# Kernel optimization log

Hardware: AMD Instinct MI355X
Metric: run time of the kernel (lower is better)

## Reference

```python
import jax, jax.numpy as jnp
import numpy as np

B, L, D, R = 8, 2048, 2048, 256
K = R if R % 2 == 1 else (R - 1 if R > 1 else 1)  # torch kernel-size rule -> 255


def setup_inputs() -> dict:
    key = jax.random.key(0)
    ks = jax.random.split(key, 6)
    x = jax.random.normal(ks[0], (B, L, D), dtype=jnp.float32)
    ln_gamma = jnp.ones((D,), jnp.float32)
    ln_beta = jnp.zeros((D,), jnp.float32)
    P_shared = jax.random.normal(ks[1], (D, R), jnp.float32) / np.float32(np.sqrt(D))
    dlt_T = jax.random.normal(ks[2], (R, R), jnp.float32) / np.float32(np.sqrt(R))
    phi_w = jax.random.normal(ks[3], (R,), jnp.float32)  # nn.Linear(1, r, bias=False) weight
    phi_bias = jnp.zeros((L, R), jnp.float32)            # created as zeros_like(phi_det)
    toep_params = jnp.ones((K,), jnp.float32) / np.float32(K)
    Wq = jax.random.normal(ks[4], (R, D), jnp.float32) / np.float32(np.sqrt(R))  # delta_Q: r->d
    bq = jnp.zeros((D,), jnp.float32)
    g_logit = jnp.array([-1.0, 0.0], jnp.float32)
    return {"x": x, "ln_gamma": ln_gamma, "ln_beta": ln_beta, "P_shared": P_shared,
            "dlt_T": dlt_T, "phi_w": phi_w, "phi_bias": phi_bias,
            "toep_params": toep_params, "Wq": Wq, "bq": bq, "g_logit": g_logit,
            "step": 5000}


def _layernorm(x, g, b, eps=1e-5):
    m = jnp.mean(x, -1, keepdims=True)
    v = jnp.mean((x - m) ** 2, -1, keepdims=True)
    return (x - m) * jax.lax.rsqrt(v + eps) * g + b


def _phi_det(Ll, Rr, dtype):
    # assumed phi_logic(t, L, r): DCT-II style deterministic phase table, shape (L, r)
    t = jnp.arange(Ll, dtype=dtype)[:, None]
    k = jnp.arange(Rr, dtype=dtype)[None, :]
    return jnp.cos(jnp.pi * (t + 0.5) * k / Ll)


def reference(x, ln_gamma, ln_beta, P_shared, dlt_T, phi_w, phi_bias,
              toep_params, Wq, bq, g_logit, step):
    Bb, Ll, Dd = x.shape
    Rr = P_shared.shape[1]
    x_norm = _layernorm(x, ln_gamma, ln_beta)
    phi_det = _phi_det(Ll, Rr, x.dtype)                      # (L, r)
    feat = jnp.mean(x_norm, -1, keepdims=True)               # (B, L, 1)
    phi_data = jnp.mean(feat * phi_w[None, None, :], axis=0)  # (L, r)
    det_scale = min(step / 2000.0, 1.0)                      # static Python scalar
    phi = det_scale * phi_det + phi_bias + phi_data          # (L, r)
    scale = jnp.sum(phi, axis=1) / jnp.float32(Rr)           # (L,)
    u = jnp.einsum('bld,dr->blr', x_norm, P_shared)          # SharedProj.forward_P
    z = jnp.einsum('blr,sr->bls', u, dlt_T)                  # DLT: fixed spectral transform
    # Toeplitz conv1d across spectral channels, padding 'same' (cross-correlation, as torch)
    zf = z.reshape(Bb * Ll, 1, Rr)
    mixed = jax.lax.conv_general_dilated(zf, toep_params[None, None, :], (1,), 'SAME',
                                         dimension_numbers=('NCH', 'OIH', 'NCH'))
    z_mixed = mixed.reshape(Bb, Ll, Rr)
    y = jnp.einsum('blr,rd->bld', z_mixed, Wq) + bq          # delta_Q
    g = jax.nn.sigmoid(g_logit)
    g = jnp.repeat(g, Dd // g.shape[0])                      # repeat_interleave to d_model
    # scale has L elements, broadcast over the FEATURE dim (L == d_model by construction)
    return g[None, None, :] * y * scale[None, None, :]
```

## Files before the change

kernel.cpp:

```cpp
#include <hip/hip_runtime.h>
#include <cstdint>
#include <math.h>

#define B_ 8
#define L_ 2048
#define D_ 2048
#define R_ 256

typedef __bf16 bf16x8 __attribute__((ext_vector_type(8)));
typedef float f32x4 __attribute__((ext_vector_type(4)));

__device__ __forceinline__ unsigned short f2bf(float f) {
    uint32_t u = __builtin_bit_cast(uint32_t, f);
    u += 0x7FFFu + ((u >> 16) & 1u);
    return (unsigned short)(u >> 16);
}

#define GLDS16(gp, lp)                                                          \
    __builtin_amdgcn_global_load_lds(                                           \
        (const __attribute__((address_space(1))) void*)(gp),                    \
        (__attribute__((address_space(3))) void*)(lp), 16, 0, 0)

__global__ __launch_bounds__(256) void ln_kernel(
    const float* __restrict__ x, const float* __restrict__ gamma,
    const float* __restrict__ beta, unsigned short* __restrict__ xn,
    float* __restrict__ feat)
{
    const int row  = blockIdx.x;
    const int t    = threadIdx.x;
    const int w    = t >> 6, lane = t & 63;
    const float4* x4 = (const float4*)(x + (size_t)row * D_);
    const float4* g4 = (const float4*)gamma;
    const float4* b4 = (const float4*)beta;
    float4 a  = x4[t];
    float4 b  = x4[t + 256];
    float4 g0 = g4[t], g1 = g4[t + 256];
    float4 e0 = b4[t], e1 = b4[t + 256];

    float s   = a.x + a.y + a.z + a.w + b.x + b.y + b.z + b.w;
    float sq  = a.x*a.x + a.y*a.y + a.z*a.z + a.w*a.w
              + b.x*b.x + b.y*b.y + b.z*b.z + b.w*b.w;
    float sxg = a.x*g0.x + a.y*g0.y + a.z*g0.z + a.w*g0.w
              + b.x*g1.x + b.y*g1.y + b.z*g1.z + b.w*g1.w;
    float sg  = g0.x + g0.y + g0.z + g0.w + g1.x + g1.y + g1.z + g1.w;
    float sb  = e0.x + e0.y + e0.z + e0.w + e1.x + e1.y + e1.z + e1.w;

    __shared__ float red[20];
#pragma unroll
    for (int o = 32; o; o >>= 1) {
        s   += __shfl_down(s, o);
        sq  += __shfl_down(sq, o);
        sxg += __shfl_down(sxg, o);
        sg  += __shfl_down(sg, o);
        sb  += __shfl_down(sb, o);
    }
    if (lane == 0) {
        red[w] = s; red[4+w] = sq; red[8+w] = sxg; red[12+w] = sg; red[16+w] = sb;
    }
    __syncthreads();
    float S    = red[0] + red[1] + red[2] + red[3];
    float SQ   = red[4] + red[5] + red[6] + red[7];
    float SXG  = red[8] + red[9] + red[10] + red[11];
    float SG   = red[12] + red[13] + red[14] + red[15];
    float SB   = red[16] + red[17] + red[18] + red[19];
    float mean = S * (1.0f / D_);
    float var  = SQ * (1.0f / D_) - mean * mean;
    float rstd = rsqrtf(var + 1e-5f);
    if (t == 0)
        feat[row] = (rstd * (SXG - mean * SG) + SB) * (1.0f / D_);

    float n[8];
    n[0] = (a.x - mean) * rstd * g0.x + e0.x;
    n[1] = (a.y - mean) * rstd * g0.y + e0.y;
    n[2] = (a.z - mean) * rstd * g0.z + e0.z;
    n[3] = (a.w - mean) * rstd * g0.w + e0.w;
    n[4] = (b.x - mean) * rstd * g1.x + e1.x;
    n[5] = (b.y - mean) * rstd * g1.y + e1.y;
    n[6] = (b.z - mean) * rstd * g1.z + e1.z;
    n[7] = (b.w - mean) * rstd * g1.w + e1.w;

    ushort4 o0, o1;
    o0.x = f2bf(n[0]); o0.y = f2bf(n[1]); o0.z = f2bf(n[2]); o0.w = f2bf(n[3]);
    o1.x = f2bf(n[4]); o1.y = f2bf(n[5]); o1.z = f2bf(n[6]); o1.w = f2bf(n[7]);
    ((ushort4*)(xn + (size_t)row * D_))[t]       = o0;
    ((ushort4*)(xn + (size_t)row * D_))[t + 256] = o1;
}

__global__ __launch_bounds__(256) void prep1_kernel(
    const float* __restrict__ P, unsigned short* __restrict__ PT,
    const float* __restrict__ toep, const float* __restrict__ Wq,
    float* __restrict__ C,
    const float* __restrict__ phi_bias, const float* __restrict__ phi_w,
    const float* __restrict__ feat, const float* __restrict__ bq,
    const float* __restrict__ g_logit, const int* __restrict__ step,
    float* __restrict__ gs, float* __restrict__ bgs)
{
    __shared__ __align__(16) char smem[32768];
    const int bid = blockIdx.x;
    const int t   = threadIdx.x;

    if (bid < 32) {
        unsigned short* sT = (unsigned short*)smem;
        const int k0 = bid * 64;
#pragma unroll 8
        for (int j = 0; j < 64; j++)
            sT[j * 256 + t] = f2bf(P[(size_t)(k0 + j) * R_ + t]);
        __syncthreads();
#pragma unroll
        for (int c = 0; c < 16; c++) {
            ushort4 v;
            v.x = sT[(c * 4 + 0) * 256 + t];
            v.y = sT[(c * 4 + 1) * 256 + t];
            v.z = sT[(c * 4 + 2) * 256 + t];
            v.w = sT[(c * 4 + 3) * 256 + t];
            *(ushort4*)(PT + (size_t)t * D_ + k0 + c * 4) = v;
        }
    } else if (bid < 160) {
        float* T2 = (float*)smem;
        const int cid = bid - 32;
        const int r0  = (cid >> 3) * 16;
        const int d   = (cid & 7) * 256 + t;
        {
            int j0 = t - 128;
            T2[t] = ((unsigned)j0 < 255u) ? toep[j0] : 0.f;
            int j1 = t + 128;
            T2[t + 256] = ((unsigned)j1 < 255u) ? toep[j1] : 0.f;
        }
        __syncthreads();
        float acc[16] = {};
#pragma unroll 4
        for (int s = 0; s < 256; s++) {
            float wv = Wq[(size_t)s * D_ + d];
            int base = r0 - s + 255;
#pragma unroll
            for (int ri = 0; ri < 16; ri++)
                acc[ri] += T2[base + ri] * wv;
        }
#pragma unroll
        for (int ri = 0; ri < 16; ri++)
            C[(size_t)(r0 + ri) * D_ + d] = acc[ri];
    } else {
        float* redp = (float*)smem;
        const int l0   = (bid - 160) * 32;
        const int w    = t >> 6, lane = t & 63;
        float pw = phi_w[t];
#pragma unroll
        for (int o = 32; o; o >>= 1) pw += __shfl_down(pw, o);
        if (lane == 0) redp[w] = pw;
        __syncthreads();
        float pws = redp[0] + redp[1] + redp[2] + redp[3];
        float det = fminf((float)step[0] / 2000.0f, 1.0f);
        float fscl = pws * (1.0f / B_);
#pragma unroll
        for (int i = 0; i < 8; i++) {
            int l = l0 + w * 8 + i;
            float4 pv = *(const float4*)(phi_bias + (size_t)l * R_ + lane * 4);
            float val = pv.x + pv.y + pv.z + pv.w;
            if (lane < 8) val += feat[(size_t)lane * L_ + l] * fscl;
#pragma unroll
            for (int o = 32; o; o >>= 1) val += __shfl_down(val, o);
            if (lane == 0) {
                float a  = 3.14159265358979323846f * ((float)l + 0.5f) * (1.0f / L_);
                float cs = sinf(128.0f * a) * cosf(127.5f * a) / sinf(0.5f * a);
                float sc = (det * cs + val) * (1.0f / R_);
                float gl = g_logit[l >> 10];
                float gg = 1.0f / (1.0f + expf(-gl));
                gs[l]  = gg * sc;
                bgs[l] = bq[l] * gg * sc;
            }
        }
    }
}

__global__ __launch_bounds__(256) void prep2_kernel(
    const float* __restrict__ dlt, const float* __restrict__ C,
    unsigned short* __restrict__ WT)
{
    const int d0 = blockIdx.x * 2;
    const int q  = threadIdx.x;
    float a0 = 0.f, a1 = 0.f;
#pragma unroll 8
    for (int r = 0; r < 256; r++) {
        float dv = dlt[(size_t)r * R_ + q];
        const float* cr = C + (size_t)r * D_ + d0;
        a0 += dv * cr[0];
        a1 += dv * cr[1];
    }
    WT[(size_t)(d0 + 0) * R_ + q] = f2bf(a0);
    WT[(size_t)(d0 + 1) * R_ + q] = f2bf(a1);
}

__global__ __launch_bounds__(256, 2) void gemm1_kernel(
    const unsigned short* __restrict__ A,
    const unsigned short* __restrict__ BT,
    unsigned short* __restrict__ U)
{
    __shared__ __align__(16) unsigned short sA[2][2][128 * 32];
    __shared__ __align__(16) unsigned short sB[2][2][128 * 32];
    const int tid  = threadIdx.x;
    const int n0   = blockIdx.x * 128;
    const int m0   = blockIdx.y * 128;
    const int w    = tid >> 6, lane = tid & 63;
    const int quad = lane >> 4, m16 = lane & 15;
    const int wm   = (w >> 1) * 64, wn = (w & 1) * 64;
    const int ra   = tid >> 2, sa = tid & 3;

    const unsigned short* apb = A  + (size_t)(m0 + ra) * 2048 + sa * 8;
    const unsigned short* bpb = BT + (size_t)(n0 + ra) * 2048 + sa * 8;

    f32x4 acc[4][4] = {};

#define G1_STAGE(buf, kc)                                                       \
    do {                                                                        \
        _Pragma("unroll")                                                       \
        for (int h = 0; h < 2; h++) {                                           \
            GLDS16(apb + (kc) + h * 32,              &sA[buf][h][tid * 8]);     \
            GLDS16(apb + (kc) + h * 32 + 64 * 2048,  &sA[buf][h][2048 + tid * 8]); \
            GLDS16(bpb + (kc) + h * 32,              &sB[buf][h][tid * 8]);     \
            GLDS16(bpb + (kc) + h * 32 + 64 * 2048,  &sB[buf][h][2048 + tid * 8]); \
        }                                                                       \
    } while (0)

    G1_STAGE(0, 0);
    __syncthreads();

    int cur = 0;
    for (int kc = 0; kc < 2048; kc += 64) {
        if (kc + 64 < 2048) G1_STAGE(cur ^ 1, kc + 64);
#pragma unroll
        for (int h = 0; h < 2; h++) {
            bf16x8 af[4], bf[4];
#pragma unroll
            for (int i = 0; i < 4; i++)
                af[i] = *(const bf16x8*)(&sA[cur][h][(wm + i * 16 + m16) * 32 + quad * 8]);
#pragma unroll
            for (int j = 0; j < 4; j++)
                bf[j] = *(const bf16x8*)(&sB[cur][h][(wn + j * 16 + m16) * 32 + quad * 8]);
#pragma unroll
            for (int i = 0; i < 4; i++)
#pragma unroll
                for (int j = 0; j < 4; j++)
                    acc[i][j] = __builtin_amdgcn_mfma_f32_16x16x32_bf16(
                        af[i], bf[j], acc[i][j], 0, 0, 0);
        }
        __syncthreads();
        cur ^= 1;
    }
#undef G1_STAGE

#pragma unroll
    for (int i = 0; i < 4; i++)
#pragma unroll
        for (int j = 0; j < 4; j++) {
            int col = n0 + wn + j * 16 + m16;
#pragma unroll
            for (int r = 0; r < 4; r++) {
                int row = m0 + wm + i * 16 + quad * 4 + r;
                U[(size_t)row * 256 + col] = f2bf(acc[i][j][r]);
            }
        }
}

__global__ __launch_bounds__(256, 3) void gemm2_kernel(
    const unsigned short* __restrict__ A,
    const unsigned short* __restrict__ BT,
    const float* __restrict__ gs, const float* __restrict__ bgs,
    float* __restrict__ out)
{
    __shared__ __align__(16) unsigned short sA[2][128 * 32];
    __shared__ __align__(16) unsigned short sB[2][128 * 32];
    const int tid  = threadIdx.x;
    const int n0   = blockIdx.x * 128;
    const int m0   = blockIdx.y * 128;
    const int w    = tid >> 6, lane = tid & 63;
    const int quad = lane >> 4, m16 = lane & 15;
    const int wm   = (w >> 1) * 64, wn = (w & 1) * 64;
    const int ra   = tid >> 2, sa = tid & 3;

    const unsigned short* apb0 = A  + (size_t)(m0 + ra) * 256 + sa * 8;
    const unsigned short* apb1 = apb0 + (size_t)64 * 256;
    const unsigned short* bpb0 = BT + (size_t)(n0 + ra) * 256 + sa * 8;
    const unsigned short* bpb1 = bpb0 + (size_t)64 * 256;

    float gv[4], bv[4];
#pragma unroll
    for (int j = 0; j < 4; j++) {
        int col = n0 + wn + j * 16 + m16;
        gv[j] = gs[col];
        bv[j] = bgs[col];
    }

    f32x4 acc[4][4] = {};

#define G2_STAGE(buf, kc)                                      \
    do {                                                       \
        GLDS16(apb0 + (kc), &sA[buf][tid * 8]);                \
        GLDS16(apb1 + (kc), &sA[buf][(256 + tid) * 8]);        \
        GLDS16(bpb0 + (kc), &sB[buf][tid * 8]);                \
        GLDS16(bpb1 + (kc), &sB[buf][(256 + tid) * 8]);        \
    } while (0)

    G2_STAGE(0, 0);
    __syncthreads();

    int cur = 0;
    for (int kc = 0; kc < 256; kc += 32) {
        if (kc + 32 < 256) G2_STAGE(cur ^ 1, kc + 32);
        bf16x8 af[4], bf[4];
#pragma unroll
        for (int i = 0; i < 4; i++)
            af[i] = *(const bf16x8*)(&sA[cur][(wm + i * 16 + m16) * 32 + quad * 8]);
#pragma unroll
        for (int j = 0; j < 4; j++)
            bf[j] = *(const bf16x8*)(&sB[cur][(wn + j * 16 + m16) * 32 + quad * 8]);
#pragma unroll
        for (int i = 0; i < 4; i++)
#pragma unroll
            for (int j = 0; j < 4; j++)
                acc[i][j] = __builtin_amdgcn_mfma_f32_16x16x32_bf16(
                    af[i], bf[j], acc[i][j], 0, 0, 0);
        __syncthreads();
        cur ^= 1;
    }
#undef G2_STAGE

#pragma unroll
    for (int i = 0; i < 4; i++)
#pragma unroll
        for (int r = 0; r < 4; r++) {
            int row = m0 + wm + i * 16 + quad * 4 + r;
            float* op = out + (size_t)row * 2048 + n0 + wn;
#pragma unroll
            for (int j = 0; j < 4; j++)
                op[j * 16 + m16] = acc[i][j][r] * gv[j] + bv[j];
        }
}

extern "C" void kernel_launch(void* const* d_in, const int* in_sizes, int n_in,
                              void* d_out, int out_size, void* d_ws, size_t ws_size,
                              hipStream_t stream)
{
    const float* x        = (const float*)d_in[0];
    const float* ln_gamma = (const float*)d_in[1];
    const float* ln_beta  = (const float*)d_in[2];
    const float* P        = (const float*)d_in[3];
    const float* dlt      = (const float*)d_in[4];
    const float* phi_w    = (const float*)d_in[5];
    const float* phi_bias = (const float*)d_in[6];
    const float* toep     = (const float*)d_in[7];
    const float* Wq       = (const float*)d_in[8];
    const float* bq       = (const float*)d_in[9];
    const float* g_logit  = (const float*)d_in[10];
    const int*   step     = (const int*)d_in[11];
    float* out = (float*)d_out;

    char* w = (char*)d_ws;
    unsigned short* xn  = (unsigned short*)(w);
    unsigned short* u   = (unsigned short*)(w + 67108864);
    unsigned short* PT  = (unsigned short*)(w + 75497472);
    unsigned short* WT  = (unsigned short*)(w + 76546048);
    float*          C   = (float*)(w + 77594624);
    float*          feat= (float*)(w + 79691776);
    float*          gs  = (float*)(w + 79757312);
    float*          bgs = (float*)(w + 79765504);

    ln_kernel<<<dim3(B_ * L_), dim3(256), 0, stream>>>(x, ln_gamma, ln_beta, xn, feat);
    prep1_kernel<<<dim3(224), dim3(256), 0, stream>>>(P, PT, toep, Wq, C,
                                                      phi_bias, phi_w, feat, bq,
                                                      g_logit, step, gs, bgs);
    prep2_kernel<<<dim3(1024), dim3(256), 0, stream>>>(dlt, C, WT);
    gemm1_kernel<<<dim3(2, 128), dim3(256), 0, stream>>>(xn, PT, u);
    gemm2_kernel<<<dim3(16, 128), dim3(256), 0, stream>>>(u, WT, gs, bgs, out);
}
```

Measured before the change: 373.4 us.

## Merge layernorm and weight-prep kernels into two multi-role launches

Folds the layernorm, the P transpose and the Toeplitz·Wq precompute into one launch, with blocks picking their role by block index. The dlt·C product and the phi/gate scale computation share a second launch. LN blocks now handle 8 rows each, so the gamma/beta loads and reductions happen once per block rather than once per row. This removes one kernel launch and lets the independent prep work run alongside the layernorm, at the cost of an extra barrier per row and less parallelism inside each LN block.

```diff
diff --git a/kernel.cpp b/kernel.cpp
--- a/kernel.cpp
+++ b/kernel.cpp
@@ -21,93 +21,92 @@
         (const __attribute__((address_space(1))) void*)(gp),                    \
         (__attribute__((address_space(3))) void*)(lp), 16, 0, 0)
 
-__global__ __launch_bounds__(256) void ln_kernel(
+__global__ __launch_bounds__(256) void fuseA_kernel(
     const float* __restrict__ x, const float* __restrict__ gamma,
     const float* __restrict__ beta, unsigned short* __restrict__ xn,
-    float* __restrict__ feat)
-{
-    const int row  = blockIdx.x;
-    const int t    = threadIdx.x;
-    const int w    = t >> 6, lane = t & 63;
-    const float4* x4 = (const float4*)(x + (size_t)row * D_);
-    const float4* g4 = (const float4*)gamma;
-    const float4* b4 = (const float4*)beta;
-    float4 a  = x4[t];
-    float4 b  = x4[t + 256];
-    float4 g0 = g4[t], g1 = g4[t + 256];
-    float4 e0 = b4[t], e1 = b4[t + 256];
-
-    float s   = a.x + a.y + a.z + a.w + b.x + b.y + b.z + b.w;
-    float sq  = a.x*a.x + a.y*a.y + a.z*a.z + a.w*a.w
-              + b.x*b.x + b.y*b.y + b.z*b.z + b.w*b.w;
-    float sxg = a.x*g0.x + a.y*g0.y + a.z*g0.z + a.w*g0.w
-              + b.x*g1.x + b.y*g1.y + b.z*g1.z + b.w*g1.w;
-    float sg  = g0.x + g0.y + g0.z + g0.w + g1.x + g1.y + g1.z + g1.w;
-    float sb  = e0.x + e0.y + e0.z + e0.w + e1.x + e1.y + e1.z + e1.w;
-
-    __shared__ float red[20];
-#pragma unroll
-    for (int o = 32; o; o >>= 1) {
-        s   += __shfl_down(s, o);
-        sq  += __shfl_down(sq, o);
-        sxg += __shfl_down(sxg, o);
-        sg  += __shfl_down(sg, o);
-        sb  += __shfl_down(sb, o);
-    }
-    if (lane == 0) {
-        red[w] = s; red[4+w] = sq; red[8+w] = sxg; red[12+w] = sg; red[16+w] = sb;
-    }
-    __syncthreads();
-    float S    = red[0] + red[1] + red[2] + red[3];
-    float SQ   = red[4] + red[5] + red[6] + red[7];
-    float SXG  = red[8] + red[9] + red[10] + red[11];
-    float SG   = red[12] + red[13] + red[14] + red[15];
-    float SB   = red[16] + red[17] + red[18] + red[19];
-    float mean = S * (1.0f / D_);
-    float var  = SQ * (1.0f / D_) - mean * mean;
-    float rstd = rsqrtf(var + 1e-5f);
-    if (t == 0)
-        feat[row] = (rstd * (SXG - mean * SG) + SB) * (1.0f / D_);
-
-    float n[8];
-    n[0] = (a.x - mean) * rstd * g0.x + e0.x;
-    n[1] = (a.y - mean) * rstd * g0.y + e0.y;
-    n[2] = (a.z - mean) * rstd * g0.z + e0.z;
-    n[3] = (a.w - mean) * rstd * g0.w + e0.w;
-    n[4] = (b.x - mean) * rstd * g1.x + e1.x;
-    n[5] = (b.y - mean) * rstd * g1.y + e1.y;
-    n[6] = (b.z - mean) * rstd * g1.z + e1.z;
-    n[7] = (b.w - mean) * rstd * g1.w + e1.w;
-
-    ushort4 o0, o1;
-    o0.x = f2bf(n[0]); o0.y = f2bf(n[1]); o0.z = f2bf(n[2]); o0.w = f2bf(n[3]);
-    o1.x = f2bf(n[4]); o1.y = f2bf(n[5]); o1.z = f2bf(n[6]); o1.w = f2bf(n[7]);
-    ((ushort4*)(xn + (size_t)row * D_))[t]       = o0;
-    ((ushort4*)(xn + (size_t)row * D_))[t + 256] = o1;
-}
-
-__global__ __launch_bounds__(256) void prep1_kernel(
+    float* __restrict__ feat,
     const float* __restrict__ P, unsigned short* __restrict__ PT,
     const float* __restrict__ toep, const float* __restrict__ Wq,
-    float* __restrict__ C,
-    const float* __restrict__ phi_bias, const float* __restrict__ phi_w,
-    const float* __restrict__ feat, const float* __restrict__ bq,
-    const float* __restrict__ g_logit, const int* __restrict__ step,
-    float* __restrict__ gs, float* __restrict__ bgs)
-{
-    __shared__ __align__(16) char smem[32768];
+    float* __restrict__ C)
+{
+    __shared__ __align__(16) char smem[16384];
     const int bid = blockIdx.x;
     const int t   = threadIdx.x;
 
-    if (bid < 32) {
+    if (bid < 2048) {
+        float* red = (float*)smem;
+        const int w = t >> 6, lane = t & 63;
+        const float4* g4 = (const float4*)gamma;
+        const float4* b4 = (const float4*)beta;
+        float4 g0 = g4[t], g1 = g4[t + 256];
+        float4 e0 = b4[t], e1 = b4[t + 256];
+
+        float sg = g0.x+g0.y+g0.z+g0.w + g1.x+g1.y+g1.z+g1.w;
+        float sb = e0.x+e0.y+e0.z+e0.w + e1.x+e1.y+e1.z+e1.w;
+#pragma unroll
+        for (int o = 32; o; o >>= 1) {
+            sg += __shfl_down(sg, o);
+            sb += __shfl_down(sb, o);
+        }
+        if (lane == 0) { red[w] = sg; red[4+w] = sb; }
+        __syncthreads();
+        const float SG = red[0] + red[1] + red[2] + red[3];
+        const float SB = red[4] + red[5] + red[6] + red[7];
+        __syncthreads();
+
+        for (int i = 0; i < 8; i++) {
+            const int row = bid * 8 + i;
+            const float4* x4 = (const float4*)(x + (size_t)row * D_);
+            float4 a = x4[t];
+            float4 b = x4[t + 256];
+
+            float s   = a.x + a.y + a.z + a.w + b.x + b.y + b.z + b.w;
+            float sq  = a.x*a.x + a.y*a.y + a.z*a.z + a.w*a.w
+                      + b.x*b.x + b.y*b.y + b.z*b.z + b.w*b.w;
+            float sxg = a.x*g0.x + a.y*g0.y + a.z*g0.z + a.w*g0.w
+                      + b.x*g1.x + b.y*g1.y + b.z*g1.z + b.w*g1.w;
+#pragma unroll
+            for (int o = 32; o; o >>= 1) {
+                s   += __shfl_down(s, o);
+                sq  += __shfl_down(sq, o);
+                sxg += __shfl_down(sxg, o);
+            }
+            if (lane == 0) { red[w] = s; red[4+w] = sq; red[8+w] = sxg; }
+            __syncthreads();
+            float S    = red[0] + red[1] + red[2] + red[3];
+            float SQ   = red[4] + red[5] + red[6] + red[7];
+            float SXG  = red[8] + red[9] + red[10] + red[11];
+            float mean = S * (1.0f / D_);
+            float var  = SQ * (1.0f / D_) - mean * mean;
+            float rstd = rsqrtf(var + 1e-5f);
+            if (t == 0)
+                feat[row] = (rstd * (SXG - mean * SG) + SB) * (1.0f / D_);
+
+            float n0 = (a.x - mean) * rstd * g0.x + e0.x;
+            float n1 = (a.y - mean) * rstd * g0.y + e0.y;
+            float n2 = (a.z - mean) * rstd * g0.z + e0.z;
+            float n3 = (a.w - mean) * rstd * g0.w + e0.w;
+            float n4 = (b.x - mean) * rstd * g1.x + e1.x;
+            float n5 = (b.y - mean) * rstd * g1.y + e1.y;
+            float n6 = (b.z - mean) * rstd * g1.z + e1.z;
+            float n7 = (b.w - mean) * rstd * g1.w + e1.w;
+
+            ushort4 o0, o1;
+            o0.x = f2bf(n0); o0.y = f2bf(n1); o0.z = f2bf(n2); o0.w = f2bf(n3);
+            o1.x = f2bf(n4); o1.y = f2bf(n5); o1.z = f2bf(n6); o1.w = f2bf(n7);
+            ((ushort4*)(xn + (size_t)row * D_))[t]       = o0;
+            ((ushort4*)(xn + (size_t)row * D_))[t + 256] = o1;
+            __syncthreads();
+        }
+    } else if (bid < 2112) {
         unsigned short* sT = (unsigned short*)smem;
-        const int k0 = bid * 64;
+        const int k0 = (bid - 2048) * 32;
 #pragma unroll 8
-        for (int j = 0; j < 64; j++)
+        for (int j = 0; j < 32; j++)
             sT[j * 256 + t] = f2bf(P[(size_t)(k0 + j) * R_ + t]);
         __syncthreads();
 #pragma unroll
-        for (int c = 0; c < 16; c++) {
+        for (int c = 0; c < 8; c++) {
             ushort4 v;
             v.x = sT[(c * 4 + 0) * 256 + t];
             v.y = sT[(c * 4 + 1) * 256 + t];
@@ -115,9 +114,9 @@
             v.w = sT[(c * 4 + 3) * 256 + t];
             *(ushort4*)(PT + (size_t)t * D_ + k0 + c * 4) = v;
         }
-    } else if (bid < 160) {
+    } else {
         float* T2 = (float*)smem;
-        const int cid = bid - 32;
+        const int cid = bid - 2112;
         const int r0  = (cid >> 3) * 16;
         const int d   = (cid & 7) * 256 + t;
         {
@@ -139,10 +138,37 @@
 #pragma unroll
         for (int ri = 0; ri < 16; ri++)
             C[(size_t)(r0 + ri) * D_ + d] = acc[ri];
+    }
+}
+
+__global__ __launch_bounds__(256) void fuseB_kernel(
+    const float* __restrict__ dlt, const float* __restrict__ C,
+    unsigned short* __restrict__ WT,
+    const float* __restrict__ phi_bias, const float* __restrict__ phi_w,
+    const float* __restrict__ feat, const float* __restrict__ bq,
+    const float* __restrict__ g_logit, const int* __restrict__ step,
+    float* __restrict__ gs, float* __restrict__ bgs)
+{
+    __shared__ float redp[4];
+    const int bid = blockIdx.x;
+    const int t   = threadIdx.x;
+
+    if (bid < 1024) {
+        const int d0 = bid * 2;
+        const int q  = t;
+        float a0 = 0.f, a1 = 0.f;
+#pragma unroll 8
+        for (int r = 0; r < 256; r++) {
+            float dv = dlt[(size_t)r * R_ + q];
+            const float* cr = C + (size_t)r * D_ + d0;
+            a0 += dv * cr[0];
+            a1 += dv * cr[1];
+        }
+        WT[(size_t)(d0 + 0) * R_ + q] = f2bf(a0);
+        WT[(size_t)(d0 + 1) * R_ + q] = f2bf(a1);
     } else {
-        float* redp = (float*)smem;
-        const int l0   = (bid - 160) * 32;
-        const int w    = t >> 6, lane = t & 63;
+        const int l0 = (bid - 1024) * 32;
+        const int w  = t >> 6, lane = t & 63;
         float pw = phi_w[t];
 #pragma unroll
         for (int o = 32; o; o >>= 1) pw += __shfl_down(pw, o);
@@ -170,24 +196,6 @@
             }
         }
     }
-}
-
-__global__ __launch_bounds__(256) void prep2_kernel(
-    const float* __restrict__ dlt, const float* __restrict__ C,
-    unsigned short* __restrict__ WT)
-{
-    const int d0 = blockIdx.x * 2;
-    const int q  = threadIdx.x;
-    float a0 = 0.f, a1 = 0.f;
-#pragma unroll 8
-    for (int r = 0; r < 256; r++) {
-        float dv = dlt[(size_t)r * R_ + q];
-        const float* cr = C + (size_t)r * D_ + d0;
-        a0 += dv * cr[0];
-        a1 += dv * cr[1];
-    }
-    WT[(size_t)(d0 + 0) * R_ + q] = f2bf(a0);
-    WT[(size_t)(d0 + 1) * R_ + q] = f2bf(a1);
 }
 
 __global__ __launch_bounds__(256, 2) void gemm1_kernel(
@@ -364,11 +372,10 @@
     float*          gs  = (float*)(w + 79757312);
     float*          bgs = (float*)(w + 79765504);
 
-    ln_kernel<<<dim3(B_ * L_), dim3(256), 0, stream>>>(x, ln_gamma, ln_beta, xn, feat);
-    prep1_kernel<<<dim3(224), dim3(256), 0, stream>>>(P, PT, toep, Wq, C,
-                                                      phi_bias, phi_w, feat, bq,
-                                                      g_logit, step, gs, bgs);
-    prep2_kernel<<<dim3(1024), dim3(256), 0, stream>>>(dlt, C, WT);
+    fuseA_kernel<<<dim3(2240), dim3(256), 0, stream>>>(x, ln_gamma, ln_beta, xn, feat,
+                                                       P, PT, toep, Wq, C);
+    fuseB_kernel<<<dim3(1088), dim3(256), 0, stream>>>(dlt, C, WT, phi_bias, phi_w,
+                                                       feat, bq, g_logit, step, gs, bgs);
     gemm1_kernel<<<dim3(2, 128), dim3(256), 0, stream>>>(xn, PT, u);
     gemm2_kernel<<<dim3(16, 128), dim3(256), 0, stream>>>(u, WT, gs, bgs, out);
 }
```

Result: slower. 398.7 us (+6.8%).
